# Optimization experiments

Measured on AMD Instinct MI355X. Metric: run time of the kernel, lower is better.

The kernel has to match this reference:

```python
import jax, jax.numpy as jnp
import numpy as np

D_MODEL = 1024
D_FF = 4096


def _layernorm(x, g, b, eps=1e-5):
    mu = jnp.mean(x, axis=-1, keepdims=True)
    var = jnp.var(x, axis=-1, keepdims=True)
    return (x - mu) * jax.lax.rsqrt(var + eps) * g + b


def setup_inputs() -> dict:
    key = jax.random.key(0)
    ks = jax.random.split(key, 16)
    d, f = D_MODEL, D_FF
    s = 1.0 / np.sqrt(d)
    inp = {
        'x': jax.random.normal(ks[0], (4, 2048, d), dtype=jnp.float32),
        'wq': jax.random.uniform(ks[1], (d, d), jnp.float32, -s, s),
        'bq': jax.random.uniform(ks[2], (d,), jnp.float32, -s, s),
        'wk': jax.random.uniform(ks[3], (d, d), jnp.float32, -s, s),
        'bk': jax.random.uniform(ks[4], (d,), jnp.float32, -s, s),
        'wv': jax.random.uniform(ks[5], (d, d), jnp.float32, -s, s),
        'bv': jax.random.uniform(ks[6], (d,), jnp.float32, -s, s),
        'wo': jax.random.uniform(ks[7], (d, d), jnp.float32, -s, s),
        'bo': jax.random.uniform(ks[8], (d,), jnp.float32, -s, s),
        'w1': jax.random.uniform(ks[9], (d, f), jnp.float32, -s, s),
        'b1': jax.random.uniform(ks[10], (f,), jnp.float32, -s, s),
        'w2': jax.random.uniform(ks[11], (f, d), jnp.float32, -1.0 / np.sqrt(f), 1.0 / np.sqrt(f)),
        'b2': jax.random.uniform(ks[12], (d,), jnp.float32, -1.0 / np.sqrt(f), 1.0 / np.sqrt(f)),
        'g1': jnp.ones((d,), jnp.float32),
        'be1': jnp.zeros((d,), jnp.float32),
        'g2': jnp.ones((d,), jnp.float32),
        'be2': jnp.zeros((d,), jnp.float32),
    }
    return inp


def reference(x, wq, bq, wk, bk, wv, bv, wo, bo, w1, b1, w2, b2, g1, be1, g2, be2):
    d_k = x.shape[-1]
    q = jnp.einsum('bsd,de->bse', x, wq) + bq
    k = jnp.einsum('bsd,de->bse', x, wk) + bk
    v = jnp.einsum('bsd,de->bse', x, wv) + bv
    # full-width attention (no head split in the original module)
    scores = jnp.einsum('bqd,bkd->bqk', q, k) / jnp.sqrt(jnp.float32(d_k))
    attn = jax.nn.softmax(scores, axis=-1)
    ctx = jnp.einsum('bqk,bkd->bqd', attn, v)
    attn_out = jnp.einsum('bsd,de->bse', ctx, wo) + bo
    x1 = _layernorm(x + attn_out, g1, be1)
    ff = jnp.einsum('bsf,fd->bsd', jax.nn.relu(jnp.einsum('bsd,df->bsf', x1, w1) + b1), w2) + b2
    return _layernorm(x1 + ff, g2, be2)
```

## Files before the change

kernel.cpp:

```cpp
#include <hip/hip_runtime.h>
#include <stdint.h>


using f32x4 = __attribute__((ext_vector_type(4))) float;
using s16x8 = __attribute__((ext_vector_type(8))) short;

__device__ __forceinline__ ushort f2b(float f) {
    union { float f; uint32_t u; } v; v.f = f;
    uint32_t u = v.u;
    return (ushort)((u + 0x7fffu + ((u >> 16) & 1u)) >> 16);
}
__device__ __forceinline__ float b2f(ushort b) {
    union { uint32_t u; float f; } v; v.u = ((uint32_t)b) << 16;
    return v.f;
}
__device__ __forceinline__ float to_f(float f) { return f; }
__device__ __forceinline__ float to_f(ushort b) { return b2f(b); }

__device__ __forceinline__ void async_ld16(const ushort* g, ushort* l) {
    __builtin_amdgcn_global_load_lds(
        (const __attribute__((address_space(1))) void*)g,
        (__attribute__((address_space(3))) void*)l,
        16, 0, 0);
}

#define WAITCNT_VM4    0x0F74
#define WAITCNT_VM0    0x0F70
#define WAITCNT_LGKM12 0xCC7F
#define WAITCNT_LGKM0  0xC07F


__global__ __launch_bounds__(256) void cast_f2b4(const float* __restrict__ src,
                                                 ushort* __restrict__ dst,
                                                 long long n4) {
    long long i = (long long)blockIdx.x * 256 + threadIdx.x;
    if (i >= n4) return;
    float4 f = ((const float4*)src)[i];
    ushort4 o;
    o.x = f2b(f.x); o.y = f2b(f.y); o.z = f2b(f.z); o.w = f2b(f.w);
    ((ushort4*)dst)[i] = o;
}


__global__ __launch_bounds__(256) void concat3(const float* __restrict__ a,
                                               const float* __restrict__ b,
                                               const float* __restrict__ c,
                                               float* __restrict__ dst) {
    int i = blockIdx.x * 256 + threadIdx.x;
    const float* s = (i < 1024) ? a : (i < 2048) ? b : c;
    dst[i] = s[i & 1023];
}


__global__ __launch_bounds__(256) void add2_cast(const float* __restrict__ a,
                                                 const float* __restrict__ b,
                                                 ushort* __restrict__ o,
                                                 long long n4) {
    long long i = (long long)blockIdx.x * 256 + threadIdx.x;
    if (i >= n4) return;
    float4 x = ((const float4*)a)[i];
    float4 y = ((const float4*)b)[i];
    ushort4 u;
    u.x = f2b(x.x + y.x); u.y = f2b(x.y + y.y);
    u.z = f2b(x.z + y.z); u.w = f2b(x.w + y.w);
    ((ushort4*)o)[i] = u;
}


template <typename T>
__global__ __launch_bounds__(256) void transpose_to_bf16(const T* __restrict__ src,
                                                         ushort* __restrict__ dst,
                                                         int R, int C, int srcLd,
                                                         long long ss, long long ds) {
    __shared__ float tile[32][33];
    src += (long long)blockIdx.z * ss;
    dst += (long long)blockIdx.z * ds;
    const int c0 = blockIdx.x * 32;
    const int r0 = blockIdx.y * 32;
    const int tx = threadIdx.x, ty = threadIdx.y;
#pragma unroll
    for (int i = 0; i < 4; i++) {
        int r = r0 + ty + i * 8;
        tile[ty + i * 8][tx] = to_f(src[(long long)r * srcLd + c0 + tx]);
    }
    __syncthreads();
#pragma unroll
    for (int i = 0; i < 4; i++) {
        int r = c0 + ty + i * 8;
        dst[(long long)r * R + r0 + tx] = f2b(tile[tx][ty + i * 8]);
    }
}


__global__ __launch_bounds__(256) void transpose4_to_bf16(const float* __restrict__ s0,
                                                          const float* __restrict__ s1,
                                                          const float* __restrict__ s2,
                                                          const float* __restrict__ s3,
                                                          ushort* __restrict__ dst) {
    __shared__ float tile[32][33];
    const int D = 1024;
    const int z = blockIdx.z;
    const float* src = (z == 0) ? s0 : (z == 1) ? s1 : (z == 2) ? s2 : s3;
    dst += (long long)z * D * D;
    const int c0 = blockIdx.x * 32;
    const int r0 = blockIdx.y * 32;
    const int tx = threadIdx.x, ty = threadIdx.y;
#pragma unroll
    for (int i = 0; i < 4; i++) {
        int r = r0 + ty + i * 8;
        tile[ty + i * 8][tx] = src[(long long)r * D + c0 + tx];
    }
    __syncthreads();
#pragma unroll
    for (int i = 0; i < 4; i++) {
        int r = c0 + ty + i * 8;
        dst[(long long)r * D + r0 + tx] = f2b(tile[tx][ty + i * 8]);
    }
}


template <int OUT_BF16, int RELU, int HAS_BIAS>
__global__ __launch_bounds__(512, 2) void gemm256(const ushort* __restrict__ A,
                                                  const ushort* __restrict__ BT,
                                                  void* __restrict__ Cp,
                                                  const float* __restrict__ bias,
                                                  int K, int kChunks, float scale,
                                                  int lda, int ldb, int ldc,
                                                  long long sA, long long sB,
                                                  long long sC, long long sK) {
    __shared__ ushort SH[65536];
    ushort* Asl = SH;
    ushort* Bsl = SH + 32768;

    const int tid = threadIdx.x;
    const int kIdx = blockIdx.z % kChunks;
    const int bz = blockIdx.z / kChunks;
    const int kLen = K / kChunks;
    const int kOff = kIdx * kLen;
    const int kTiles = kLen >> 5;
    const ushort* Ab = A + (long long)bz * sA;
    const ushort* Bb = BT + (long long)bz * sB;

    const int W = gridDim.x, H = gridDim.y;
    const int bidx = blockIdx.y * W + blockIdx.x;
    const int Hp = H >> 3;
    const int xcd = bidx & 7;
    const int sb = bidx >> 3;
    const int tn = sb / Hp;
    const int tm = xcd * Hp + sb % Hp;

    const int lane = tid & 63;
    const int w = tid >> 6;
    const int wm = w >> 2;
    const int wn = w & 3;
    const int l16 = lane & 15;
    const int quad = lane >> 4;

    const int lr = lane >> 2;
    const int lc = ((lane & 3) ^ ((lane >> 3) & 3)) * 8;
    const ushort* AgS = Ab + (long long)(tm * 256 + w * 32 + lr) * lda + kOff + lc;
    const ushort* BgS = Bb + (long long)(tn * 256 + w * 32 + lr) * ldb + kOff + lc;
    ushort* AsW = Asl + w * 1024;
    ushort* BsW = Bsl + w * 1024;
    const long long rstepA = (long long)16 * lda;
    const long long rstepB = (long long)16 * ldb;

#define STG(tt) { const int bf_ = (tt) & 3;                                       \
        const ushort* ga_ = AgS + (tt) * 32; const ushort* gb_ = BgS + (tt) * 32; \
        async_ld16(ga_, AsW + bf_ * 8192);                                        \
        async_ld16(ga_ + rstepA, AsW + bf_ * 8192 + 512);                         \
        async_ld16(gb_, BsW + bf_ * 8192);                                        \
        async_ld16(gb_ + rstepB, BsW + bf_ * 8192 + 512); }

    const int fsl = (quad ^ ((l16 >> 1) & 3)) * 8;
    const ushort* ArdB = Asl + (wm * 128 + l16) * 32 + fsl;
    const ushort* BrdB = Bsl + (wn * 64 + l16) * 32 + fsl;

#define LDF(pre, tt) { const int bf_ = (tt) & 3;                                  \
        const ushort* Ar_ = ArdB + bf_ * 8192;                                    \
        const ushort* Br_ = BrdB + bf_ * 8192;                                    \
        _Pragma("unroll") for (int i_ = 0; i_ < 8; i_++)                          \
            pre##a[i_] = *(const s16x8*)(Ar_ + i_ * 512);                         \
        _Pragma("unroll") for (int j_ = 0; j_ < 4; j_++)                          \
            pre##b[j_] = *(const s16x8*)(Br_ + j_ * 512); }

#define MM(pre) {                                                                 \
        __builtin_amdgcn_sched_barrier(0);                                        \
        __builtin_amdgcn_s_setprio(1);                                            \
        _Pragma("unroll") for (int i_ = 0; i_ < 8; i_++)                          \
            _Pragma("unroll") for (int j_ = 0; j_ < 4; j_++)                      \
                acc[i_][j_] = __builtin_amdgcn_mfma_f32_16x16x32_bf16(            \
                    pre##a[i_], pre##b[j_], acc[i_][j_], 0, 0, 0);                \
        __builtin_amdgcn_s_setprio(0);                                            \
        __builtin_amdgcn_sched_barrier(0); }

    f32x4 acc[8][4];
#pragma unroll
    for (int i = 0; i < 8; i++)
#pragma unroll
        for (int j = 0; j < 4; j++) acc[i][j] = (f32x4){0.f, 0.f, 0.f, 0.f};

    s16x8 fca[8], fna[8];
    s16x8 fcb[4], fnb[4];

    STG(0); STG(1); STG(2);
    __builtin_amdgcn_s_waitcnt(WAITCNT_VM4);
    __builtin_amdgcn_s_barrier();
    LDF(fc, 0);

    for (int t = 0; t < kTiles; t += 2) {
        if (t + 1 < kTiles) LDF(fn, t + 1);
        if (t + 3 < kTiles) STG(t + 3);
        if (t + 1 < kTiles) __builtin_amdgcn_s_waitcnt(WAITCNT_LGKM12);
        else                __builtin_amdgcn_s_waitcnt(WAITCNT_LGKM0);
        MM(fc);
        if (t + 2 < kTiles) {
            if (t + 3 < kTiles) __builtin_amdgcn_s_waitcnt(WAITCNT_VM4);
            else                __builtin_amdgcn_s_waitcnt(WAITCNT_VM0);
            __builtin_amdgcn_s_barrier();
        }
        if (t + 1 < kTiles) {
            if (t + 2 < kTiles) LDF(fc, t + 2);
            if (t + 4 < kTiles) STG(t + 4);
            if (t + 2 < kTiles) __builtin_amdgcn_s_waitcnt(WAITCNT_LGKM12);
            else                __builtin_amdgcn_s_waitcnt(WAITCNT_LGKM0);
            MM(fn);
            if (t + 3 < kTiles) {
                if (t + 4 < kTiles) __builtin_amdgcn_s_waitcnt(WAITCNT_VM4);
                else                __builtin_amdgcn_s_waitcnt(WAITCNT_VM0);
                __builtin_amdgcn_s_barrier();
            }
        }
    }
#undef STG
#undef LDF
#undef MM

    __builtin_amdgcn_s_barrier();

    const long long cb = (long long)bz * sC + (long long)kIdx * sK;
    if (OUT_BF16) {
        ushort* Cb = (ushort*)Cp;
#pragma unroll
        for (int j = 0; j < 4; j++) {
            const int cg = wn * 4 + j;
            const float bv = HAS_BIAS ? bias[tn * 256 + cg * 16 + l16] : 0.0f;
#pragma unroll
            for (int i = 0; i < 8; i++) {
                const int rbase = wm * 128 + i * 16 + quad * 4;
#pragma unroll
                for (int r = 0; r < 4; r++) {
                    const int row = rbase + r;
                    float v = acc[i][j][r] * scale + bv;
                    if (RELU) v = v > 0.f ? v : 0.f;
                    SH[row * 256 + ((cg ^ ((row >> 2) & 3)) << 4) + l16] = f2b(v);
                }
            }
        }
        __builtin_amdgcn_s_barrier();
        const int crow = tid >> 5;
        const int cch = tid & 31;
        const int g = cch >> 1, hh = cch & 1;
#pragma unroll
        for (int pass = 0; pass < 16; pass++) {
            const int row = pass * 16 + crow;
            s16x8 vv = *(const s16x8*)&SH[row * 256 + ((g ^ ((row >> 2) & 3)) << 4) + hh * 8];
            *(s16x8*)&Cb[cb + (long long)(tm * 256 + row) * ldc + tn * 256 + cch * 8] = vv;
        }
    } else {
        float* Cf = (float*)Cp;
        float* SHf = (float*)SH;
#pragma unroll
        for (int half = 0; half < 2; half++) {
            if (wm == half) {
#pragma unroll
                for (int j = 0; j < 4; j++) {
                    const int col = wn * 64 + j * 16 + l16;
                    const float bv = (HAS_BIAS && kIdx == 0) ? bias[tn * 256 + col] : 0.0f;
                    const int gg = col >> 3, cl = col & 7;
#pragma unroll
                    for (int i = 0; i < 8; i++) {
                        const int rbase = i * 16 + quad * 4;
#pragma unroll
                        for (int r = 0; r < 4; r++) {
                            const int row = rbase + r;
                            float v = acc[i][j][r] * scale + bv;
                            if (RELU) v = v > 0.f ? v : 0.f;
                            SHf[row * 256 + ((gg ^ ((row >> 2) & 3)) << 3) + cl] = v;
                        }
                    }
                }
            }
            __builtin_amdgcn_s_barrier();
            const int rr = tid >> 6, cc = tid & 63;
            const int g2 = cc >> 1, h2 = cc & 1;
#pragma unroll
            for (int pass = 0; pass < 16; pass++) {
                const int row = pass * 8 + rr;
                f32x4 vv = *(const f32x4*)&SHf[row * 256 + ((g2 ^ ((row >> 2) & 3)) << 3) + h2 * 4];
                *(f32x4*)&Cf[cb + (long long)(tm * 256 + half * 128 + row) * ldc + tn * 256 + cc * 4] = vv;
            }
            __builtin_amdgcn_s_barrier();
        }
    }
}


__global__ __launch_bounds__(256) void softmax_rows(const ushort* __restrict__ S,
                                                    ushort* __restrict__ P) {
    const int C = 2048;
    const long long row = blockIdx.x;
    const int tid = threadIdx.x;
    const ushort4* s4 = (const ushort4*)(S + row * C) + tid * 2;
    ushort4 a = s4[0], bq = s4[1];
    float v[8];
    v[0] = b2f(a.x); v[1] = b2f(a.y); v[2] = b2f(a.z); v[3] = b2f(a.w);
    v[4] = b2f(bq.x); v[5] = b2f(bq.y); v[6] = b2f(bq.z); v[7] = b2f(bq.w);
    float mx = -1e30f;
#pragma unroll
    for (int i = 0; i < 8; i++) mx = fmaxf(mx, v[i]);
    __shared__ float red[256];
    red[tid] = mx;
    __syncthreads();
    for (int off = 128; off > 0; off >>= 1) {
        if (tid < off) red[tid] = fmaxf(red[tid], red[tid + off]);
        __syncthreads();
    }
    mx = red[0];
    __syncthreads();
    float sum = 0.f;
#pragma unroll
    for (int i = 0; i < 8; i++) {
        v[i] = __expf(v[i] - mx);
        sum += v[i];
    }
    red[tid] = sum;
    __syncthreads();
    for (int off = 128; off > 0; off >>= 1) {
        if (tid < off) red[tid] += red[tid + off];
        __syncthreads();
    }
    float inv = 1.f / red[0];
    ushort4 o0, o1;
    o0.x = f2b(v[0] * inv); o0.y = f2b(v[1] * inv); o0.z = f2b(v[2] * inv); o0.w = f2b(v[3] * inv);
    o1.x = f2b(v[4] * inv); o1.y = f2b(v[5] * inv); o1.z = f2b(v[6] * inv); o1.w = f2b(v[7] * inv);
    ushort4* p4 = (ushort4*)(P + row * C) + tid * 2;
    p4[0] = o0;
    p4[1] = o1;
}


__global__ __launch_bounds__(256) void residual_ln(const float* __restrict__ X,
                                                   const float* __restrict__ Y,
                                                   const float* __restrict__ Y2,
                                                   const float* __restrict__ g,
                                                   const float* __restrict__ be,
                                                   float* __restrict__ outf,
                                                   ushort* __restrict__ outb) {
    const int D = 1024;
    const long long row = blockIdx.x;
    const float* x = X + row * D;
    const float* y = Y + row * D;
    const float* y2 = Y2 ? Y2 + row * D : nullptr;
    const int tid = threadIdx.x;
    float v[4];
    float s = 0.f, s2 = 0.f;
#pragma unroll
    for (int i = 0; i < 4; i++) {
        int c = tid + i * 256;
        float t = x[c] + y[c];
        if (y2) t += y2[c];
        v[i] = t;
        s += t;
        s2 += t * t;
    }
    __shared__ float r1[256], r2[256];
    r1[tid] = s;
    r2[tid] = s2;
    __syncthreads();
    for (int off = 128; off > 0; off >>= 1) {
        if (tid < off) {
            r1[tid] += r1[tid + off];
            r2[tid] += r2[tid + off];
        }
        __syncthreads();
    }
    float mu = r1[0] * (1.f / 1024.f);
    float var = r2[0] * (1.f / 1024.f) - mu * mu;
    float inv = rsqrtf(var + 1e-5f);
    float* of = outf + row * D;
    ushort* ob = outb ? outb + row * D : nullptr;
#pragma unroll
    for (int i = 0; i < 4; i++) {
        int c = tid + i * 256;
        float o = (v[i] - mu) * inv * g[c] + be[c];
        of[c] = o;
        if (ob) ob[c] = f2b(o);
    }
}


extern "C" void kernel_launch(void* const* d_in, const int* in_sizes, int n_in,
                              void* d_out, int out_size, void* d_ws, size_t ws_size,
                              hipStream_t stream) {
    const float* x  = (const float*)d_in[0];
    const float* wq = (const float*)d_in[1];
    const float* bq = (const float*)d_in[2];
    const float* wk = (const float*)d_in[3];
    const float* bk = (const float*)d_in[4];
    const float* wv = (const float*)d_in[5];
    const float* bv = (const float*)d_in[6];
    const float* wo = (const float*)d_in[7];
    const float* bo = (const float*)d_in[8];
    const float* w1 = (const float*)d_in[9];
    const float* b1 = (const float*)d_in[10];
    const float* w2 = (const float*)d_in[11];
    const float* b2 = (const float*)d_in[12];
    const float* g1 = (const float*)d_in[13];
    const float* be1 = (const float*)d_in[14];
    const float* g2 = (const float*)d_in[15];
    const float* be2 = (const float*)d_in[16];
    float* out = (float*)d_out;
    char* ws = (char*)d_ws;

    const int Bz = 4, S = 2048, D = 1024, F = 4096;
    const int T = Bz * S;
    const size_t MBy = 1024ull * 1024ull;

    ushort* qkvT = (ushort*)(ws + 0);
    ushort* woT  = (ushort*)(ws + 6 * MBy);
    ushort* w1T  = (ushort*)(ws + 8 * MBy);
    ushort* w2T  = (ushort*)(ws + 16 * MBy);
    float*  bqkv = (float*)(ws + 24 * MBy);
    ushort* xb   = (ushort*)(ws + 25 * MBy);
    ushort* qkv  = (ushort*)(ws + 41 * MBy);
    ushort* vT   = (ushort*)(ws + 89 * MBy);
    ushort* scb  = (ushort*)(ws + 105 * MBy);
    ushort* attn = (ushort*)(ws + 169 * MBy);
    float*  ctx0 = (float*)(ws + 105 * MBy);
    float*  ctx1 = (float*)(ws + 137 * MBy);
    ushort* ctxb = (ushort*)(ws + 25 * MBy);
    float*  ao0 = (float*)(ws + 105 * MBy);
    float*  ao1 = (float*)(ws + 137 * MBy);
    float*  x1  = (float*)(ws + 41 * MBy);
    ushort* x1b = (ushort*)(ws + 73 * MBy);
    ushort* h   = (ushort*)(ws + 105 * MBy);
    float*  ff0 = (float*)(ws + 169 * MBy);
    float*  ff1 = (float*)(ws + 73 * MBy);

    dim3 b32(32, 8);

    cast_f2b4<<<(T * D) / 1024, 256, 0, stream>>>(x, xb, (long long)(T * D) / 4);

    transpose4_to_bf16<<<dim3(32, 32, 4), b32, 0, stream>>>(wq, wk, wv, wo, qkvT);
    transpose_to_bf16<float><<<dim3(128, 32, 1), b32, 0, stream>>>(w1, w1T, D, F, F, 0, 0);
    transpose_to_bf16<float><<<dim3(32, 128, 1), b32, 0, stream>>>(w2, w2T, F, D, D, 0, 0);

    concat3<<<12, 256, 0, stream>>>(bq, bk, bv, bqkv);

    gemm256<1, 0, 1><<<dim3(3 * D / 256, T / 256, 1), 512, 0, stream>>>(
        xb, qkvT, qkv, bqkv, D, 1, 1.f, D, D, 3 * D, 0, 0, 0, 0);

    transpose_to_bf16<ushort><<<dim3(D / 32, S / 32, Bz), b32, 0, stream>>>(
        qkv + 2048, vT, S, D, 3 * D, (long long)S * 3 * D, (long long)S * D);

    gemm256<1, 0, 0><<<dim3(S / 256, S / 256, Bz), 512, 0, stream>>>(
        qkv, qkv + 1024, scb, nullptr, D, 1, 0.03125f, 3 * D, 3 * D, S,
        (long long)S * 3 * D, (long long)S * 3 * D, (long long)S * S, 0);

    softmax_rows<<<T, 256, 0, stream>>>(scb, attn);

    gemm256<0, 0, 0><<<dim3(D / 256, S / 256, Bz * 2), 512, 0, stream>>>(
        attn, vT, ctx0, nullptr, S, 2, 1.f, S, S, D,
        (long long)S * S, (long long)D * S, (long long)S * D, (long long)(ctx1 - ctx0));

    add2_cast<<<(T * D) / 1024, 256, 0, stream>>>(ctx0, ctx1, ctxb, (long long)(T * D) / 4);

    gemm256<0, 0, 1><<<dim3(D / 256, T / 256, 2), 512, 0, stream>>>(
        ctxb, woT, ao0, bo, D, 2, 1.f, D, D, D, 0, 0, 0, (long long)(ao1 - ao0));

    residual_ln<<<T, 256, 0, stream>>>(x, ao0, ao1, g1, be1, x1, x1b);

    gemm256<1, 1, 1><<<dim3(F / 256, T / 256, 1), 512, 0, stream>>>(
        x1b, w1T, h, b1, D, 1, 1.f, D, D, F, 0, 0, 0, 0);

    gemm256<0, 0, 1><<<dim3(D / 256, T / 256, 2), 512, 0, stream>>>(
        h, w2T, ff0, b2, F, 2, 1.f, F, F, D, 0, 0, 0, (long long)(ff1 - ff0));

    residual_ln<<<T, 256, 0, stream>>>(x1, ff0, ff1, g2, be2, out, nullptr);
}
```

Before: 567.7 us.

## Restructure GEMM main loop into ping-pong half-tile phases with split A/B staging

Replaces the double-buffered register-fragment loop (full LDF of 8 A plus 4 B fragments, then 32 MFMAs) with a phase schedule. Each k-tile is split into two halves of 16 MFMAs each, and the A and B global-to-LDS async loads are interleaved between them, with barriers around each phase. This lowers register pressure for fragments and spreads memory issue to overlap with MFMA work, but it adds many more barriers per tile and drops the next-tile LDS prefetch overlap. It also assumes an even number of k-tiles, at least four, with four LDS buffers.

```diff
diff --git a/kernel.cpp b/kernel.cpp
--- a/kernel.cpp
+++ b/kernel.cpp
@@ -26,7 +26,6 @@
 
 #define WAITCNT_VM4    0x0F74
 #define WAITCNT_VM0    0x0F70
-#define WAITCNT_LGKM12 0xCC7F
 #define WAITCNT_LGKM0  0xC07F
 
 
@@ -165,34 +164,57 @@
     const long long rstepA = (long long)16 * lda;
     const long long rstepB = (long long)16 * ldb;
 
-#define STG(tt) { const int bf_ = (tt) & 3;                                       \
-        const ushort* ga_ = AgS + (tt) * 32; const ushort* gb_ = BgS + (tt) * 32; \
-        async_ld16(ga_, AsW + bf_ * 8192);                                        \
-        async_ld16(ga_ + rstepA, AsW + bf_ * 8192 + 512);                         \
-        async_ld16(gb_, BsW + bf_ * 8192);                                        \
-        async_ld16(gb_ + rstepB, BsW + bf_ * 8192 + 512); }
+#define STG_AU(tt, boff) { const ushort* ga_ = AgS + (tt) * 32;                   \
+        async_ld16(ga_, AsW + (boff));                                            \
+        async_ld16(ga_ + rstepA, AsW + (boff) + 512); }
+#define STG_BU(tt, boff) { const ushort* gb_ = BgS + (tt) * 32;                   \
+        async_ld16(gb_, BsW + (boff));                                            \
+        async_ld16(gb_ + rstepB, BsW + (boff) + 512); }
 
     const int fsl = (quad ^ ((l16 >> 1) & 3)) * 8;
     const ushort* ArdB = Asl + (wm * 128 + l16) * 32 + fsl;
     const ushort* BrdB = Bsl + (wn * 64 + l16) * 32 + fsl;
 
-#define LDF(pre, tt) { const int bf_ = (tt) & 3;                                  \
-        const ushort* Ar_ = ArdB + bf_ * 8192;                                    \
-        const ushort* Br_ = BrdB + bf_ * 8192;                                    \
-        _Pragma("unroll") for (int i_ = 0; i_ < 8; i_++)                          \
-            pre##a[i_] = *(const s16x8*)(Ar_ + i_ * 512);                         \
-        _Pragma("unroll") for (int j_ = 0; j_ < 4; j_++)                          \
-            pre##b[j_] = *(const s16x8*)(Br_ + j_ * 512); }
-
-#define MM(pre) {                                                                 \
-        __builtin_amdgcn_sched_barrier(0);                                        \
-        __builtin_amdgcn_s_setprio(1);                                            \
-        _Pragma("unroll") for (int i_ = 0; i_ < 8; i_++)                          \
-            _Pragma("unroll") for (int j_ = 0; j_ < 4; j_++)                      \
-                acc[i_][j_] = __builtin_amdgcn_mfma_f32_16x16x32_bf16(            \
-                    pre##a[i_], pre##b[j_], acc[i_][j_], 0, 0, 0);                \
-        __builtin_amdgcn_s_setprio(0);                                            \
-        __builtin_amdgcn_sched_barrier(0); }
+#define LDA4(dst, boff, ib) {                                                     \
+    _Pragma("unroll") for (int i_ = 0; i_ < 4; i_++)                              \
+        dst[i_] = *(const s16x8*)(ArdB + (boff) + ((ib) + i_) * 512); }
+#define LDB4(boff) {                                                              \
+    _Pragma("unroll") for (int j_ = 0; j_ < 4; j_++)                              \
+        fb[j_] = *(const s16x8*)(BrdB + (boff) + j_ * 512); }
+#define MM16(asrc, io) {                                                          \
+    _Pragma("unroll") for (int i_ = 0; i_ < 4; i_++)                              \
+    _Pragma("unroll") for (int j_ = 0; j_ < 4; j_++)                              \
+        acc[(io) + i_][j_] = __builtin_amdgcn_mfma_f32_16x16x32_bf16(             \
+            asrc[i_], fb[j_], acc[(io) + i_][j_], 0, 0, 0); }
+
+#define BAR   __builtin_amdgcn_s_barrier()
+#define PRIO1 __builtin_amdgcn_s_setprio(1)
+#define PRIO0 __builtin_amdgcn_s_setprio(0)
+#define WVM4  __builtin_amdgcn_s_waitcnt(WAITCNT_VM4)
+#define WVM0  __builtin_amdgcn_s_waitcnt(WAITCNT_VM0)
+#define WLG0  __builtin_amdgcn_s_waitcnt(WAITCNT_LGKM0)
+
+#define PAIR(c0, c1, d0, d1, t2, t3, LAST) {                                      \
+                               \
+    LDA4(fa, c0, 0); LDB4(c0);                                                    \
+    if (!(LAST)) STG_AU(t2, d0);                                                  \
+    BAR; WLG0; PRIO1; MM16(fa, 0); PRIO0; BAR;                                    \
+     \
+    LDA4(fa2, c0, 4);                                                             \
+    if (!(LAST)) STG_BU(t2, d0);                                                  \
+    BAR; WLG0; PRIO1; MM16(fa2, 4); PRIO0;                                        \
+    if (LAST) { WVM0; } else { WVM4; }                                            \
+    BAR;                                                                          \
+                               \
+    LDA4(fa, c1, 0); LDB4(c1);                                                    \
+    if (!(LAST)) STG_AU(t3, d1);                                                  \
+    BAR; WLG0; PRIO1; MM16(fa, 0); PRIO0; BAR;                                    \
+     \
+    LDA4(fa2, c1, 4);                                                             \
+    if (!(LAST)) STG_BU(t3, d1);                                                  \
+    BAR; WLG0; PRIO1; MM16(fa2, 4); PRIO0;                                        \
+    if (!(LAST)) { WVM4; }                                                        \
+    BAR; }
 
     f32x4 acc[8][4];
 #pragma unroll
@@ -200,43 +222,29 @@
 #pragma unroll
         for (int j = 0; j < 4; j++) acc[i][j] = (f32x4){0.f, 0.f, 0.f, 0.f};
 
-    s16x8 fca[8], fna[8];
-    s16x8 fcb[4], fnb[4];
-
-    STG(0); STG(1); STG(2);
-    __builtin_amdgcn_s_waitcnt(WAITCNT_VM4);
-    __builtin_amdgcn_s_barrier();
-    LDF(fc, 0);
-
-    for (int t = 0; t < kTiles; t += 2) {
-        if (t + 1 < kTiles) LDF(fn, t + 1);
-        if (t + 3 < kTiles) STG(t + 3);
-        if (t + 1 < kTiles) __builtin_amdgcn_s_waitcnt(WAITCNT_LGKM12);
-        else                __builtin_amdgcn_s_waitcnt(WAITCNT_LGKM0);
-        MM(fc);
-        if (t + 2 < kTiles) {
-            if (t + 3 < kTiles) __builtin_amdgcn_s_waitcnt(WAITCNT_VM4);
-            else                __builtin_amdgcn_s_waitcnt(WAITCNT_VM0);
-            __builtin_amdgcn_s_barrier();
-        }
-        if (t + 1 < kTiles) {
-            if (t + 2 < kTiles) LDF(fc, t + 2);
-            if (t + 4 < kTiles) STG(t + 4);
-            if (t + 2 < kTiles) __builtin_amdgcn_s_waitcnt(WAITCNT_LGKM12);
-            else                __builtin_amdgcn_s_waitcnt(WAITCNT_LGKM0);
-            MM(fn);
-            if (t + 3 < kTiles) {
-                if (t + 4 < kTiles) __builtin_amdgcn_s_waitcnt(WAITCNT_VM4);
-                else                __builtin_amdgcn_s_waitcnt(WAITCNT_VM0);
-                __builtin_amdgcn_s_barrier();
-            }
-        }
-    }
-#undef STG
-#undef LDF
-#undef MM
-
-    __builtin_amdgcn_s_barrier();
+    s16x8 fa[4], fa2[4], fb[4];
+
+    STG_AU(0, 0); STG_BU(0, 0); STG_AU(1, 8192); STG_BU(1, 8192);
+    WVM4;
+    BAR;
+
+    const int nP = kTiles >> 1;
+    int pr = 0;
+    for (; pr + 3 <= nP; pr += 2) {
+        PAIR(0, 8192, 16384, 24576, 2 * pr + 2, 2 * pr + 3, 0);
+        PAIR(16384, 24576, 0, 8192, 2 * pr + 4, 2 * pr + 5, 0);
+    }
+    PAIR(0, 8192, 16384, 24576, 2 * pr + 2, 2 * pr + 3, 0);
+    PAIR(16384, 24576, 0, 8192, 0, 0, 1);
+
+#undef STG_AU
+#undef STG_BU
+#undef LDA4
+#undef LDB4
+#undef MM16
+#undef PAIR
+
+    BAR;
 
     const long long cb = (long long)bz * sC + (long long)kIdx * sK;
     if (OUT_BF16) {
@@ -257,7 +265,7 @@
                 }
             }
         }
-        __builtin_amdgcn_s_barrier();
+        BAR;
         const int crow = tid >> 5;
         const int cch = tid & 31;
         const int g = cch >> 1, hh = cch & 1;
@@ -291,7 +299,7 @@
                     }
                 }
             }
-            __builtin_amdgcn_s_barrier();
+            BAR;
             const int rr = tid >> 6, cc = tid & 63;
             const int g2 = cc >> 1, h2 = cc & 1;
 #pragma unroll
@@ -300,9 +308,15 @@
                 f32x4 vv = *(const f32x4*)&SHf[row * 256 + ((g2 ^ ((row >> 2) & 3)) << 3) + h2 * 4];
                 *(f32x4*)&Cf[cb + (long long)(tm * 256 + half * 128 + row) * ldc + tn * 256 + cc * 4] = vv;
             }
-            __builtin_amdgcn_s_barrier();
+            BAR;
         }
     }
+#undef BAR
+#undef PRIO1
+#undef PRIO0
+#undef WVM4
+#undef WVM0
+#undef WLG0
 }
 
 
```

Result: faster. 553.4 us (-2.5%).
